# Performance work log

Measured on AMD Instinct MI355X. Metric: run time of the kernel, lower is better.

## Reference

```python
import jax, jax.numpy as jnp
import numpy as np

B, N, DE, H, DH = 2, 1024, 1024, 16, 64
DK = H * DH  # total complex qkv dim per stream
MIN_EXP = -30.0
EPS = 1e-4


def setup_inputs():
    key = jax.random.key(0)
    ks = jax.random.split(key, 8)

    def g(i, shape, sc=1.0):
        return jax.random.normal(ks[i], shape, jnp.float32) * sc

    # RoPE-style per-head frequencies for the conjugate-paired half-dims
    freqs = 10000.0 ** (-np.arange(DH // 2, dtype=np.float64) / (DH // 2))
    omega = jnp.asarray(np.tile(freqs[None, :], (H, 1)), jnp.float32)
    return {
        "x": g(0, (B, N, DE)),
        "Wq": g(1, (DE, 2 * DK), 1.0 / np.sqrt(DE)),
        "Wk": g(2, (DE, 2 * DK), 1.0 / np.sqrt(DE)),
        "Wv": g(3, (DE, 2 * DK), 1.0 / np.sqrt(DE)),
        "Wo": g(4, (2 * DK, DE), 1.0 / np.sqrt(2 * DK)),
        "omega": omega,
        "mu_raw": g(5, (H,)) - 2.0,          # pre-sigmoid decay rates
        "sigma_raw": g(6, (H,)),              # pre-softplus process noise
        "eta_raw": jnp.ones((H,), jnp.float32),
        "gamma_raw": jnp.ones((H,), jnp.float32),
        "tau": jnp.ones((H,), jnp.float32),   # inverse temperature
        "nu_raw": jnp.ones((H,), jnp.float32) * 4.0,  # robustness dof
    }


def reference(x, Wq, Wk, Wv, Wo, omega, mu_raw, sigma_raw, eta_raw, gamma_raw, tau, nu_raw):
    B_, N_, _ = x.shape
    H_, d_half = omega.shape
    DH_ = 2 * d_half
    DKt = H_ * DH_

    def cproj(W):
        z = x @ W                          # [B,N,2D] real/imag packed
        D = W.shape[1] // 2
        zc = jax.lax.complex(z[..., :D], z[..., D:])
        return zc.reshape(B_, N_, H_, DH_)

    q, k, v = cproj(Wq), cproj(Wk), cproj(Wv)

    # complex-conjugate-constrained rotations: omega stacked as [w, -w]
    om = jnp.concatenate([omega, -omega], axis=-1)              # [H,DH]
    t = jnp.arange(N_, dtype=jnp.float32)
    ang = t[:, None, None] * om[None]                           # [N,H,DH]
    phase = jax.lax.complex(jnp.cos(ang), jnp.sin(ang))
    qr = q * phase[None]
    kr = k * phase[None]

    # isotropic SDE decay kernel  E_rel = exp(-mu * |t_i - t_j|)
    mu = jax.nn.sigmoid(mu_raw) + EPS                           # [H]
    dt = jnp.abs(t[:, None] - t[None, :])                       # [N,N]
    E = jnp.exp(jnp.clip(-mu[:, None, None] * dt[None], MIN_EXP, 0.0))  # [H,N,N]

    # Re<q_i, Phi(dt) k_j>  (rotation carried by phases, decay by E)
    s = jnp.einsum('bihd,bjhd->bhij', qr, jnp.conj(kr)).real    # [B,H,N,N]
    qn = (q.real ** 2 + q.imag ** 2).sum(-1).transpose(0, 2, 1)  # [B,H,N]
    kn = (k.real ** 2 + k.imag ** 2).sum(-1).transpose(0, 2, 1)

    # Lyapunov-propagated uncertainty: P(dt) = sigma^2/(2mu)(1 - E^2) + eta^2 + gamma^2
    sigma_sq = jax.nn.softplus(sigma_raw)
    eta_sq = jax.nn.softplus(eta_raw)
    gamma_sq = jax.nn.softplus(gamma_raw)
    V = (sigma_sq / (2.0 * mu))[:, None, None] * (1.0 - E * E) \
        + (eta_sq + gamma_sq)[:, None, None]                    # [H,N,N]

    # per-head Mahalanobis residual under the SDE forecast
    maha = jnp.maximum(qn[..., None] + (E * E)[None] * kn[:, :, None, :]
                       - 2.0 * E[None] * s, 0.0) / V[None]      # [B,H,N,N]

    # robust nu-thresholding (Student-t style) + Gaussian normalization term
    nu = jax.nn.softplus(nu_raw)
    coef = (-0.5 * tau * (nu + DH_))[None, :, None, None]
    logits = coef * jnp.log1p(maha / nu[None, :, None, None]) \
             - 0.5 * DH_ * jnp.log(V)[None]

    causal = (t[:, None] >= t[None, :])
    logits = jnp.where(causal[None, None], logits, -jnp.inf)
    A = jax.nn.softmax(logits, axis=-1)                         # [B,H,N,N]

    out = jnp.einsum('bhij,bjhd->bihd', A.astype(v.dtype), v)   # complex [B,N,H,DH]
    y = jnp.concatenate([out.real.reshape(B_, N_, DKt),
                         out.imag.reshape(B_, N_, DKt)], axis=-1)
    return y @ Wo                                               # [B,N,DE]
```

## Files before the change

kernel.cpp:

```cpp
#include <hip/hip_runtime.h>
#include <math.h>

#define BB      2
#define NN      1024
#define DE_     1024
#define HH      16
#define TWO_DK  2048
#define PK      4194304
#define TBLR    1092

typedef float f32x4  __attribute__((ext_vector_type(4)));
typedef short bf16x8 __attribute__((ext_vector_type(8)));

__device__ __forceinline__ short f2bf(float f) {
    unsigned u = __float_as_uint(f);
    unsigned r = (u + 0x7fffu + ((u >> 16) & 1u)) >> 16;
    return (short)r;
}

#define GLDS16(g, l) __builtin_amdgcn_global_load_lds(                        \
    (const __attribute__((address_space(1))) unsigned int*)(g),               \
    (__attribute__((address_space(3))) unsigned int*)(l), 16, 0, 0)
#define GLDS4(g, l) __builtin_amdgcn_global_load_lds(                         \
    (const __attribute__((address_space(1))) unsigned int*)(g),               \
    (__attribute__((address_space(3))) unsigned int*)(l), 4, 0, 0)

__global__ __launch_bounds__(256) void prep(
    const float* __restrict__ x,
    const float* __restrict__ Wq, const float* __restrict__ Wk,
    const float* __restrict__ Wv, const float* __restrict__ Wo,
    const float* __restrict__ mu_raw, const float* __restrict__ sigma_raw,
    const float* __restrict__ eta_raw, const float* __restrict__ gamma_raw,
    short* __restrict__ xb, short* __restrict__ wt, short* __restrict__ wot,
    float4* __restrict__ tbl) {
    const int z = blockIdx.z;
    if (z == 4) {
        const int flat = blockIdx.y * 32 + blockIdx.x;
        const int i = (flat * 256 + threadIdx.x) * 8;
        float4 v0 = *(const float4*)&x[i];
        float4 v1 = *(const float4*)&x[i + 4];
        short4 o0, o1;
        o0.x = f2bf(v0.x); o0.y = f2bf(v0.y); o0.z = f2bf(v0.z); o0.w = f2bf(v0.w);
        o1.x = f2bf(v1.x); o1.y = f2bf(v1.y); o1.z = f2bf(v1.z); o1.w = f2bf(v1.w);
        *(short4*)&xb[i] = o0; *(short4*)&xb[i + 4] = o1;
        return;
    }
    if (z == 3 && blockIdx.x >= 16) {
        const int idx = blockIdx.y * 16 + (blockIdx.x - 16);
        if (idx >= 80) return;
        const int h = idx / 5, rb = idx % 5;
        const int r = rb * 256 + threadIdx.x;
        if (r >= TBLR) return;
        const float mu = 1.f / (1.f + expf(-mu_raw[h])) + 1e-4f;
        const float Ac = log1pf(expf(sigma_raw[h])) / (2.f * mu);
        const float Cc = log1pf(expf(eta_raw[h])) + log1pf(expf(gamma_raw[h]));
        const float arg = fminf(fmaxf(-mu * (float)(r - 64), -30.f), 0.f);
        const float E   = expf(arg);
        const float V   = fmaf(Ac, 1.f - E * E, Cc);
        tbl[h * TBLR + r] = make_float4(E, 1.f / V, -32.f * logf(V), 0.f);
        return;
    }
    const float* in; short* out; int R, C;
    if (z < 3) { if (blockIdx.y >= 16) return;
                 in = (z == 0) ? Wq : (z == 1) ? Wk : Wv;
                 out = wt + (size_t)z * 2097152; R = 1024; C = 2048; }
    else       { in = Wo; out = wot; R = 2048; C = 1024; }
    __shared__ float t[64][65];
    const int c0 = blockIdx.x * 64, r0 = blockIdx.y * 64;
    const int tr = threadIdx.x >> 4, tc4 = (threadIdx.x & 15) * 4;
#pragma unroll
    for (int s = 0; s < 4; ++s) {
        const int r = tr + s * 16;
        float4 v = *(const float4*)&in[(size_t)(r0 + r) * C + c0 + tc4];
        t[r][tc4] = v.x; t[r][tc4 + 1] = v.y; t[r][tc4 + 2] = v.z; t[r][tc4 + 3] = v.w;
    }
    __syncthreads();
#pragma unroll
    for (int s = 0; s < 4; ++s) {
        const int oc = tr + s * 16;
        short4 o;
        o.x = f2bf(t[tc4 + 0][oc]); o.y = f2bf(t[tc4 + 1][oc]);
        o.z = f2bf(t[tc4 + 2][oc]); o.w = f2bf(t[tc4 + 3][oc]);
        *(short4*)&out[(size_t)(c0 + oc) * R + r0 + tc4] = o;
    }
}

__global__ __launch_bounds__(256) void gemm_qkv_rot2(
    const short* __restrict__ A, const short* __restrict__ wt,
    const float* __restrict__ omega,
    short* __restrict__ qb, short* __restrict__ kb, short* __restrict__ vtb,
    float* __restrict__ qn_, float* __restrict__ kn_) {
    __shared__ __align__(16) short As[128 * 64];
    __shared__ __align__(16) short Bs[128 * 64];
    __shared__ float sN[2][128];
    const int tid = threadIdx.x;
    const int m0  = blockIdx.x * 128;
    const int h   = blockIdx.y;
    const short* W = wt + (size_t)blockIdx.z * 2097152;

    const short* aP[4]; const short* bP[4]; int ldsoff[4];
#pragma unroll
    for (int i = 0; i < 4; ++i) {
        const int c   = i * 256 + tid;
        const int row = c >> 3;
        const int src = ((c & 7) ^ (row & 7)) << 3;
        ldsoff[i] = c * 8;
        aP[i] = A + (size_t)(m0 + row) * 1024 + src;
        const int t_ = row >> 5, u_ = (row >> 4) & 1, dcol = t_ * 16 + (row & 15);
        bP[i] = W + (size_t)(u_ * 1024 + h * 64 + dcol) * 1024 + src;
    }

    const int lane = tid & 63, w = tid >> 6;
    const int wr = (w >> 1) * 64, hsel = w & 1, wc = hsel * 64;
    const int fr = lane & 15;
    const int fo = (lane >> 4) << 3;
    const int sw = (fr & 7) << 3;

    f32x4 acc[4][4];
#pragma unroll
    for (int a = 0; a < 4; ++a)
#pragma unroll
        for (int b = 0; b < 4; ++b) acc[a][b] = (f32x4){0.f, 0.f, 0.f, 0.f};

    for (int k0 = 0; k0 < 1024; k0 += 64) {
#pragma unroll
        for (int i = 0; i < 4; ++i) GLDS16(aP[i] + k0, &As[ldsoff[i]]);
#pragma unroll
        for (int i = 0; i < 4; ++i) GLDS16(bP[i] + k0, &Bs[ldsoff[i]]);
        __syncthreads();
#pragma unroll
        for (int ks = 0; ks < 64; ks += 32) {
            bf16x8 af[4], bf[4];
#pragma unroll
            for (int a = 0; a < 4; ++a)
                af[a] = *(const bf16x8*)&As[(wr + a * 16 + fr) * 64 + ((ks + fo) ^ sw)];
#pragma unroll
            for (int b = 0; b < 4; ++b)
                bf[b] = *(const bf16x8*)&Bs[(wc + b * 16 + fr) * 64 + ((ks + fo) ^ sw)];
#pragma unroll
            for (int a = 0; a < 4; ++a)
#pragma unroll
                for (int b = 0; b < 4; ++b)
                    acc[a][b] = __builtin_amdgcn_mfma_f32_16x16x32_bf16(
                        af[a], bf[b], acc[a][b], 0, 0, 0);
        }
        __syncthreads();
    }

    const int cq = (lane >> 4) * 4, l15 = lane & 15;
    const int bh  = (m0 >> 10) * 16 + h;
    const int nb0 = (m0 & 1023) + wr + cq;

    if (blockIdx.z == 2) {
#pragma unroll
        for (int a = 0; a < 4; ++a) {
#pragma unroll
            for (int b = 0; b < 4; ++b) {
                const int cl = wc + b * 16;
                const int dd = ((cl >> 4) & 1) * 64 + (cl >> 5) * 16 + l15;
                short4 o;
                o.x = f2bf(acc[a][b][0]); o.y = f2bf(acc[a][b][1]);
                o.z = f2bf(acc[a][b][2]); o.w = f2bf(acc[a][b][3]);
                *(short4*)&vtb[((size_t)bh * 128 + dd) * 1024 + nb0 + a * 16] = o;
            }
        }
        return;
    }
    float* nout = (blockIdx.z == 0) ? qn_ : kn_;
    short* obuf = (blockIdx.z == 0) ? qb  : kb;

#pragma unroll
    for (int a = 0; a < 4; ++a) {
        float ns[4] = {0.f, 0.f, 0.f, 0.f};
#pragma unroll
        for (int b = 0; b < 4; ++b)
#pragma unroll
            for (int r = 0; r < 4; ++r)
                ns[r] = fmaf(acc[a][b][r], acc[a][b][r], ns[r]);
#pragma unroll
        for (int m2 = 1; m2 < 16; m2 <<= 1)
#pragma unroll
            for (int r = 0; r < 4; ++r) ns[r] += __shfl_xor(ns[r], m2);
        if (l15 == 0)
#pragma unroll
            for (int r = 0; r < 4; ++r) sN[hsel][wr + a * 16 + cq + r] = ns[r];
    }
    __syncthreads();
    if (tid < 128)
        nout[(size_t)bh * 1024 + (m0 & 1023) + tid] = sN[0][tid] + sN[1][tid];

#pragma unroll
    for (int p = 0; p < 2; ++p) {
        const int d = (hsel * 2 + p) * 16 + l15;
        const float om = (d < 32) ? omega[h * 32 + d] : -omega[h * 32 + d - 32];
#pragma unroll
        for (int a = 0; a < 4; ++a) {
#pragma unroll
            for (int r = 0; r < 4; ++r) {
                const int n2 = nb0 + a * 16 + r;
                float sn, cs;
                __sincosf((float)n2 * om, &sn, &cs);
                const float re = acc[a][2 * p][r], im = acc[a][2 * p + 1][r];
                short* orow = obuf + ((size_t)bh * 1024 + n2) * 128;
                orow[d]      = f2bf(re * cs - im * sn);
                orow[64 + d] = f2bf(re * sn + im * cs);
            }
        }
    }
}

__global__ __launch_bounds__(256) void attn_mfma(
    const short* __restrict__ qr, const short* __restrict__ kr,
    const short* __restrict__ vt,
    const float* __restrict__ qn, const float* __restrict__ kn,
    const float4* __restrict__ tbl,
    const float* __restrict__ tau_p, const float* __restrict__ nu_raw,
    short* __restrict__ y) {
    __shared__ __align__(16) short Ks[2][64 * 128];
    __shared__ __align__(16) short Vs[2][128 * 64];
    __shared__ __align__(16) short Ps[64 * 72];
    __shared__ __align__(16) float4 sT[2][128];
    __shared__ float sKn[2][64];

    const int bx  = blockIdx.x;
    const int xcd = bx & 7;
    const int j   = bx >> 3;
    const int bh  = xcd * 4 + (j & 3);
    const int h   = bh & 15;
    const int itr = j >> 2;
    const int it  = (itr < 8) ? itr : 23 - itr;
    const int i0  = it * 64;
    const int tid  = threadIdx.x;
    const int lane = tid & 63, w = tid >> 6;
    const int quad = lane >> 4, l15 = lane & 15;

    const float nu     = log1pf(expf(nu_raw[h]));
    const float coef   = -0.5f * tau_p[h] * (nu + 64.0f);
    const float inv_nu = 1.f / nu;

    const short* Qb  = qr + (size_t)bh * NN * 128;
    const short* Kb  = kr + (size_t)bh * NN * 128;
    const short* Vtb = vt + (size_t)bh * 128 * NN;

#define STAGE(JT, P) do {                                                     \
        const int j0_ = (JT) * 64, dt0_ = i0 - j0_;                           \
        _Pragma("unroll")                                                     \
        for (int i_ = 0; i_ < 4; ++i_) {                                      \
            const int c_ = i_ * 256 + tid, row_ = c_ >> 4;                    \
            const int src_ = ((c_ & 15) ^ (row_ & 7)) * 8;                    \
            GLDS16(Kb + (size_t)(j0_ + row_) * 128 + src_, &Ks[P][c_ * 8]);   \
        }                                                                     \
        _Pragma("unroll")                                                     \
        for (int i_ = 0; i_ < 4; ++i_) {                                      \
            const int c_ = i_ * 256 + tid, d_ = c_ >> 3;                      \
            const int src_ = ((c_ & 7) ^ (d_ & 7)) * 8;                       \
            GLDS16(Vtb + (size_t)d_ * NN + j0_ + src_, &Vs[P][c_ * 8]);       \
        }                                                                     \
        if (w == 0) {                                                         \
            GLDS16(tbl + h * TBLR + 1 + dt0_ + lane, &sT[P][lane]);           \
            GLDS16(tbl + h * TBLR + 65 + dt0_ + lane, &sT[P][64 + lane]);     \
        } else if (w == 1) {                                                  \
            GLDS4(kn + (size_t)bh * NN + j0_ + lane, &sKn[P][lane]);          \
        }                                                                     \
    } while (0)

    bf16x8 qf[4];
    const int arow = i0 + w * 16 + l15;
#pragma unroll
    for (int ks = 0; ks < 4; ++ks)
        qf[ks] = *(const bf16x8*)&Qb[(size_t)arow * 128 + ks * 32 + quad * 8];

    float mrow[4], lrow[4];
    f32x4 o[8];
#pragma unroll
    for (int r = 0; r < 4; ++r) { mrow[r] = -INFINITY; lrow[r] = 0.f; }
#pragma unroll
    for (int s = 0; s < 8; ++s) o[s] = (f32x4){0.f, 0.f, 0.f, 0.f};
    float qn4[4];
#pragma unroll
    for (int r = 0; r < 4; ++r)
        qn4[r] = qn[(size_t)bh * NN + i0 + w * 16 + quad * 4 + r];

    STAGE(0, 0);
    __syncthreads();

    for (int jt = 0; jt <= it; ++jt) {
        const int p = jt & 1;
        if (jt < it) STAGE(jt + 1, 1 - p);

        f32x4 sAcc[4];
#pragma unroll
        for (int s = 0; s < 4; ++s) sAcc[s] = (f32x4){0.f, 0.f, 0.f, 0.f};
#pragma unroll
        for (int ks = 0; ks < 4; ++ks) {
#pragma unroll
            for (int s = 0; s < 4; ++s) {
                const int brow = s * 16 + l15;
                bf16x8 bK = *(const bf16x8*)&Ks[p][brow * 128 +
                                                  (((ks * 4 + quad) ^ (brow & 7)) * 8)];
                sAcc[s] = __builtin_amdgcn_mfma_f32_16x16x32_bf16(qf[ks], bK, sAcc[s], 0, 0, 0);
            }
        }

        float al[4];
#pragma unroll
        for (int r = 0; r < 4; ++r) {
            const int row = w * 16 + quad * 4 + r;
            float lg[4];
            float mx = -INFINITY;
#pragma unroll
            for (int s = 0; s < 4; ++s) {
                const int col = s * 16 + l15;
                const float4 T = sT[p][row - col + 63];
                const float sv = sAcc[s][r];
                const float maha =
                    fmaxf(fmaf(T.x * T.x, sKn[p][col], qn4[r]) - 2.f * T.x * sv, 0.f) * T.y;
                float v = fmaf(coef, __logf(fmaf(maha, inv_nu, 1.f)), T.z);
                if (jt == it && col > row) v = -INFINITY;
                lg[s] = v;
                mx = fmaxf(mx, v);
            }
            mx = fmaxf(mx, __shfl_xor(mx, 1));
            mx = fmaxf(mx, __shfl_xor(mx, 2));
            mx = fmaxf(mx, __shfl_xor(mx, 4));
            mx = fmaxf(mx, __shfl_xor(mx, 8));
            const float mn = fmaxf(mrow[r], mx);
            const float a_ = __expf(mrow[r] - mn);
            float rs = 0.f;
#pragma unroll
            for (int s = 0; s < 4; ++s) {
                const float pv = __expf(lg[s] - mn);
                Ps[row * 72 + s * 16 + l15] = f2bf(pv);
                rs += pv;
            }
            rs += __shfl_xor(rs, 1);
            rs += __shfl_xor(rs, 2);
            rs += __shfl_xor(rs, 4);
            rs += __shfl_xor(rs, 8);
            lrow[r] = fmaf(lrow[r], a_, rs);
            mrow[r] = mn;
            al[r] = a_;
        }
#pragma unroll
        for (int s = 0; s < 8; ++s)
#pragma unroll
            for (int r = 0; r < 4; ++r) o[s][r] *= al[r];

#pragma unroll
        for (int jc = 0; jc < 2; ++jc) {
            bf16x8 aP = *(const bf16x8*)&Ps[(w * 16 + l15) * 72 + jc * 32 + quad * 8];
#pragma unroll
            for (int sub = 0; sub < 8; ++sub) {
                const int d = sub * 16 + l15;
                bf16x8 bV = *(const bf16x8*)&Vs[p][d * 64 + (((jc * 4 + quad) ^ (d & 7)) * 8)];
                o[sub] = __builtin_amdgcn_mfma_f32_16x16x32_bf16(aP, bV, o[sub], 0, 0, 0);
            }
        }
        if (jt < it) __syncthreads();
    }
#undef STAGE

#pragma unroll
    for (int r = 0; r < 4; ++r) {
        const float inv = 1.f / lrow[r];
        const size_t base = ((size_t)bh * NN + i0 + w * 16 + quad * 4 + r) * 128;
#pragma unroll
        for (int sub = 0; sub < 8; ++sub)
            y[base + sub * 16 + l15] = f2bf(o[sub][r] * inv);
    }
}

__global__ __launch_bounds__(256) void gemm_out64(
    const short* __restrict__ yb, const short* __restrict__ wot,
    float* __restrict__ out) {
    __shared__ __align__(16) short As[64 * 64];
    __shared__ __align__(16) short Bs[64 * 64];
    const int tid = threadIdx.x;
    const int m0  = blockIdx.x * 64;
    const int n0  = blockIdx.y * 64;
    const int bb  = m0 >> 10;

    int aPre[2], aOff[2]; const short* bP[2];
#pragma unroll
    for (int i = 0; i < 2; ++i) {
        const int c = i * 256 + tid, row = c >> 3;
        const int src = ((c & 7) ^ (row & 7)) << 3;
        aPre[i] = ((m0 & 1023) + row) * 128 + src;
        bP[i] = wot + (size_t)(n0 + row) * 2048 + src;
        aOff[i] = c * 8;
    }

    const int lane = tid & 63, w = tid >> 6;
    const int wr = (w >> 1) * 32, wc = (w & 1) * 32;
    const int fr = lane & 15;
    const int fo = (lane >> 4) << 3;
    const int sw = (fr & 7) << 3;

    f32x4 acc[2][2];
#pragma unroll
    for (int a = 0; a < 2; ++a)
#pragma unroll
        for (int b = 0; b < 2; ++b) acc[a][b] = (f32x4){0.f, 0.f, 0.f, 0.f};

    for (int k0 = 0; k0 < 2048; k0 += 64) {
        const int hh = (k0 >> 6) & 15, im = k0 >> 10;
        const short* ab = yb + ((size_t)(bb * 16 + hh) << 17) + im * 64;
#pragma unroll
        for (int i = 0; i < 2; ++i) GLDS16(ab + aPre[i], &As[aOff[i]]);
#pragma unroll
        for (int i = 0; i < 2; ++i) GLDS16(bP[i] + k0, &Bs[aOff[i]]);
        __syncthreads();
#pragma unroll
        for (int ks = 0; ks < 64; ks += 32) {
            bf16x8 af[2], bf[2];
#pragma unroll
            for (int a = 0; a < 2; ++a)
                af[a] = *(const bf16x8*)&As[(wr + a * 16 + fr) * 64 + ((ks + fo) ^ sw)];
#pragma unroll
            for (int b = 0; b < 2; ++b)
                bf[b] = *(const bf16x8*)&Bs[(wc + b * 16 + fr) * 64 + ((ks + fo) ^ sw)];
#pragma unroll
            for (int a = 0; a < 2; ++a)
#pragma unroll
                for (int b = 0; b < 2; ++b)
                    acc[a][b] = __builtin_amdgcn_mfma_f32_16x16x32_bf16(
                        af[a], bf[b], acc[a][b], 0, 0, 0);
        }
        __syncthreads();
    }

    const int cq = (lane >> 4) * 4, l15 = lane & 15;
#pragma unroll
    for (int a = 0; a < 2; ++a)
#pragma unroll
        for (int b = 0; b < 2; ++b)
#pragma unroll
            for (int r = 0; r < 4; ++r)
                out[(size_t)(m0 + wr + a * 16 + cq + r) * 1024 +
                    (n0 + wc + b * 16 + l15)] = acc[a][b][r];
}

extern "C" void kernel_launch(void* const* d_in, const int* in_sizes, int n_in,
                              void* d_out, int out_size, void* d_ws, size_t ws_size,
                              hipStream_t stream) {
    const float* x         = (const float*)d_in[0];
    const float* Wq        = (const float*)d_in[1];
    const float* Wk        = (const float*)d_in[2];
    const float* Wv        = (const float*)d_in[3];
    const float* Wo        = (const float*)d_in[4];
    const float* omega     = (const float*)d_in[5];
    const float* mu_raw    = (const float*)d_in[6];
    const float* sigma_raw = (const float*)d_in[7];
    const float* eta_raw   = (const float*)d_in[8];
    const float* gamma_raw = (const float*)d_in[9];
    const float* tau       = (const float*)d_in[10];
    const float* nu_raw    = (const float*)d_in[11];
    float* out = (float*)d_out;

    short*  qb  = (short*)d_ws;
    short*  kb  = qb + PK;
    short*  vtb = kb + PK;
    float*  qn  = (float*)(vtb + PK);
    float*  kn  = qn + 32768;
    float4* tbl = (float4*)(kn + 32768);
    short*  wot = (short*)(tbl + HH * TBLR);
    short*  wt  = wot + 2097152;
    short*  xb  = wt + 3 * 2097152;
    short*  yb  = wt;

    prep<<<dim3(32, 32, 5), 256, 0, stream>>>(
        x, Wq, Wk, Wv, Wo, mu_raw, sigma_raw, eta_raw, gamma_raw,
        xb, wt, wot, tbl);
    gemm_qkv_rot2<<<dim3(16, 16, 3), 256, 0, stream>>>(
        xb, wt, omega, qb, kb, vtb, qn, kn);
    attn_mfma<<<dim3(512), 256, 0, stream>>>(
        qb, kb, vtb, qn, kn, tbl, tau, nu_raw, yb);
    gemm_out64<<<dim3(32, 16), 256, 0, stream>>>(yb, wot, out);
}
```

Baseline: 216.7 us.

## Pair high and low 32-row query tiles per attention block for causal balance

Each attention block now handles two 32-row query tiles, one near the end of the sequence and its mirror near the start, packed into the 64-row MFMA layout. The goal is to even out causal work across blocks so they all run a similar number of key tiles, instead of relying on the earlier tile-order permutation. Rows from the low tile stop their softmax updates once past their causal range and write zeros into P. The MFMA work on those wasted rows is still issued, and the table staging and masking logic become more complex.

```diff
diff --git a/kernel.cpp b/kernel.cpp
--- a/kernel.cpp
+++ b/kernel.cpp
@@ -219,7 +219,7 @@
     __shared__ __align__(16) short Ks[2][64 * 128];
     __shared__ __align__(16) short Vs[2][128 * 64];
     __shared__ __align__(16) short Ps[64 * 72];
-    __shared__ __align__(16) float4 sT[2][128];
+    __shared__ __align__(16) float4 sT[2][192];
     __shared__ float sKn[2][64];
 
     const int bx  = blockIdx.x;
@@ -228,11 +228,19 @@
     const int bh  = xcd * 4 + (j & 3);
     const int h   = bh & 15;
     const int itr = j >> 2;
-    const int it  = (itr < 8) ? itr : 23 - itr;
-    const int i0  = it * 64;
+    const int fi  = (itr < 8) ? itr : 23 - itr;
+    const int i0h = (31 - fi) * 32;
+    const int i0l = fi * 32;
+    const int jtHi = (31 - fi) >> 1;
+    const int jtLo = fi >> 1;
+
     const int tid  = threadIdx.x;
     const int lane = tid & 63, w = tid >> 6;
     const int quad = lane >> 4, l15 = lane & 15;
+    const int hi   = (quad < 2);
+    const int lrg  = w * 8 + (quad & 1) * 4;
+    const int i0g  = hi ? i0h : i0l;
+    const int goff = hi ? 0 : 96;
 
     const float nu     = log1pf(expf(nu_raw[h]));
     const float coef   = -0.5f * tau_p[h] * (nu + 64.0f);
@@ -243,7 +251,7 @@
     const short* Vtb = vt + (size_t)bh * 128 * NN;
 
 #define STAGE(JT, P) do {                                                     \
-        const int j0_ = (JT) * 64, dt0_ = i0 - j0_;                           \
+        const int j0_ = (JT) * 64;                                            \
         _Pragma("unroll")                                                     \
         for (int i_ = 0; i_ < 4; ++i_) {                                      \
             const int c_ = i_ * 256 + tid, row_ = c_ >> 4;                    \
@@ -257,15 +265,22 @@
             GLDS16(Vtb + (size_t)d_ * NN + j0_ + src_, &Vs[P][c_ * 8]);       \
         }                                                                     \
         if (w == 0) {                                                         \
-            GLDS16(tbl + h * TBLR + 1 + dt0_ + lane, &sT[P][lane]);           \
-            GLDS16(tbl + h * TBLR + 65 + dt0_ + lane, &sT[P][64 + lane]);     \
+            const float4* tb_ = tbl + h * TBLR + 1 + i0h - j0_;               \
+            GLDS16(tb_ + lane, &sT[P][lane]);                                 \
+            if (lane < 32) GLDS16(tb_ + 64 + lane, &sT[P][64 + lane]);        \
         } else if (w == 1) {                                                  \
+            if ((JT) <= jtLo) {                                               \
+                const float4* tb_ = tbl + h * TBLR + 1 + i0l - j0_;           \
+                GLDS16(tb_ + lane, &sT[P][96 + lane]);                        \
+                if (lane < 32) GLDS16(tb_ + 64 + lane, &sT[P][160 + lane]);   \
+            }                                                                 \
+        } else if (w == 2) {                                                  \
             GLDS4(kn + (size_t)bh * NN + j0_ + lane, &sKn[P][lane]);          \
         }                                                                     \
     } while (0)
 
     bf16x8 qf[4];
-    const int arow = i0 + w * 16 + l15;
+    const int arow = (l15 < 8) ? (i0h + w * 8 + l15) : (i0l + w * 8 + (l15 - 8));
 #pragma unroll
     for (int ks = 0; ks < 4; ++ks)
         qf[ks] = *(const bf16x8*)&Qb[(size_t)arow * 128 + ks * 32 + quad * 8];
@@ -279,14 +294,14 @@
     float qn4[4];
 #pragma unroll
     for (int r = 0; r < 4; ++r)
-        qn4[r] = qn[(size_t)bh * NN + i0 + w * 16 + quad * 4 + r];
+        qn4[r] = qn[(size_t)bh * NN + i0g + lrg + r];
 
     STAGE(0, 0);
     __syncthreads();
 
-    for (int jt = 0; jt <= it; ++jt) {
+    for (int jt = 0; jt <= jtHi; ++jt) {
         const int p = jt & 1;
-        if (jt < it) STAGE(jt + 1, 1 - p);
+        if (jt < jtHi) STAGE(jt + 1, 1 - p);
 
         f32x4 sAcc[4];
 #pragma unroll
@@ -303,43 +318,60 @@
         }
 
         float al[4];
-#pragma unroll
-        for (int r = 0; r < 4; ++r) {
-            const int row = w * 16 + quad * 4 + r;
-            float lg[4];
-            float mx = -INFINITY;
-#pragma unroll
-            for (int s = 0; s < 4; ++s) {
-                const int col = s * 16 + l15;
-                const float4 T = sT[p][row - col + 63];
-                const float sv = sAcc[s][r];
-                const float maha =
-                    fmaxf(fmaf(T.x * T.x, sKn[p][col], qn4[r]) - 2.f * T.x * sv, 0.f) * T.y;
-                float v = fmaf(coef, __logf(fmaf(maha, inv_nu, 1.f)), T.z);
-                if (jt == it && col > row) v = -INFINITY;
-                lg[s] = v;
-                mx = fmaxf(mx, v);
+        if (hi || jt <= jtLo) {
+            const int lastT = hi ? (jt == jtHi) : (jt == jtLo);
+            const int dt0g  = i0g - jt * 64;
+#pragma unroll
+            for (int r = 0; r < 4; ++r) {
+                const int prow  = w * 16 + quad * 4 + r;
+                const int lrowg = lrg + r;
+                float lg[4];
+                float mx = -INFINITY;
+#pragma unroll
+                for (int s = 0; s < 4; ++s) {
+                    const int scol = s * 16 + l15;
+                    const float4 T = sT[p][goff + lrowg - scol + 63];
+                    const float sv = sAcc[s][r];
+                    const float maha =
+                        fmaxf(fmaf(T.x * T.x, sKn[p][scol], qn4[r]) - 2.f * T.x * sv, 0.f) * T.y;
+                    float v = fmaf(coef, __logf(fmaf(maha, inv_nu, 1.f)), T.z);
+                    if (lastT && scol > dt0g + lrowg) v = -INFINITY;
+                    lg[s] = v;
+                    mx = fmaxf(mx, v);
+                }
+                mx = fmaxf(mx, __shfl_xor(mx, 1));
+                mx = fmaxf(mx, __shfl_xor(mx, 2));
+                mx = fmaxf(mx, __shfl_xor(mx, 4));
+                mx = fmaxf(mx, __shfl_xor(mx, 8));
+                const float mn = fmaxf(mrow[r], mx);
+                const float a_ = __expf(mrow[r] - mn);
+                float rs = 0.f;
+#pragma unroll
+                for (int s = 0; s < 4; ++s) {
+                    const float pv = __expf(lg[s] - mn);
+                    Ps[prow * 72 + s * 16 + l15] = f2bf(pv);
+                    rs += pv;
+                }
+                rs += __shfl_xor(rs, 1);
+                rs += __shfl_xor(rs, 2);
+                rs += __shfl_xor(rs, 4);
+                rs += __shfl_xor(rs, 8);
+                lrow[r] = fmaf(lrow[r], a_, rs);
+                mrow[r] = mn;
+                al[r] = a_;
             }
-            mx = fmaxf(mx, __shfl_xor(mx, 1));
-            mx = fmaxf(mx, __shfl_xor(mx, 2));
-            mx = fmaxf(mx, __shfl_xor(mx, 4));
-            mx = fmaxf(mx, __shfl_xor(mx, 8));
-            const float mn = fmaxf(mrow[r], mx);
-            const float a_ = __expf(mrow[r] - mn);
-            float rs = 0.f;
-#pragma unroll
-            for (int s = 0; s < 4; ++s) {
-                const float pv = __expf(lg[s] - mn);
-                Ps[row * 72 + s * 16 + l15] = f2bf(pv);
-                rs += pv;
+        } else {
+#pragma unroll
+            for (int r = 0; r < 4; ++r) al[r] = 1.f;
+            if (jt == jtLo + 1) {
+#pragma unroll
+                for (int r = 0; r < 4; ++r) {
+                    const int prow = w * 16 + quad * 4 + r;
+#pragma unroll
+                    for (int s = 0; s < 4; ++s)
+                        Ps[prow * 72 + s * 16 + l15] = 0;
+                }
             }
-            rs += __shfl_xor(rs, 1);
-            rs += __shfl_xor(rs, 2);
-            rs += __shfl_xor(rs, 4);
-            rs += __shfl_xor(rs, 8);
-            lrow[r] = fmaf(lrow[r], a_, rs);
-            mrow[r] = mn;
-            al[r] = a_;
         }
 #pragma unroll
         for (int s = 0; s < 8; ++s)
@@ -356,14 +388,14 @@
                 o[sub] = __builtin_amdgcn_mfma_f32_16x16x32_bf16(aP, bV, o[sub], 0, 0, 0);
             }
         }
-        if (jt < it) __syncthreads();
+        if (jt < jtHi) __syncthreads();
     }
 #undef STAGE
 
 #pragma unroll
     for (int r = 0; r < 4; ++r) {
         const float inv = 1.f / lrow[r];
-        const size_t base = ((size_t)bh * NN + i0 + w * 16 + quad * 4 + r) * 128;
+        const size_t base = ((size_t)bh * NN + i0g + lrg + r) * 128;
 #pragma unroll
         for (int sub = 0; sub < 8; ++sub)
             y[base + sub * 16 + l15] = f2bf(o[sub][r] * inv);
```

Measured after the change: 223.5 us. +3.2%, slower.

## Use base-2 softmax with lazy rescaling and MFMA row sums in attention

Applied to the files above, without the earlier changes.

Moves the attention logits and softmax into the base-2 domain using hardware exp2/log2 intrinsics. The table now stores 2E and E² so the Mahalanobis term needs fewer multiplies. The running max is only rescaled when it grows by more than 16, which skips most output rescales. Row sums come from an extra MFMA against a ones vector instead of shuffle reductions. The block-to-(head, tile) mapping also changes, which alters how causal work is balanced across workgroups. The trade-off is an extra MFMA per chunk and larger unnormalised probability values stored in bf16.

```diff
diff --git a/kernel.cpp b/kernel.cpp
--- a/kernel.cpp
+++ b/kernel.cpp
@@ -17,6 +17,9 @@
     unsigned r = (u + 0x7fffu + ((u >> 16) & 1u)) >> 16;
     return (short)r;
 }
+
+__device__ __forceinline__ float fexp2(float x) { return __builtin_amdgcn_exp2f(x); }
+__device__ __forceinline__ float flog2(float x) { return __builtin_amdgcn_logf(x); }
 
 #define GLDS16(g, l) __builtin_amdgcn_global_load_lds(                        \
     (const __attribute__((address_space(1))) unsigned int*)(g),               \
@@ -57,7 +60,7 @@
         const float arg = fminf(fmaxf(-mu * (float)(r - 64), -30.f), 0.f);
         const float E   = expf(arg);
         const float V   = fmaf(Ac, 1.f - E * E, Cc);
-        tbl[h * TBLR + r] = make_float4(E, 1.f / V, -32.f * logf(V), 0.f);
+        tbl[h * TBLR + r] = make_float4(2.f * E, 1.f / V, -32.f * log2f(V), E * E);
         return;
     }
     const float* in; short* out; int R, C;
@@ -225,11 +228,13 @@
     const int bx  = blockIdx.x;
     const int xcd = bx & 7;
     const int j   = bx >> 3;
-    const int bh  = xcd * 4 + (j & 3);
+    const int b2  = j & 3;
+    const int itr = j >> 2;
+    const int bh  = xcd * 4 + (b2 & 1) * 2 + (itr >> 3);
     const int h   = bh & 15;
-    const int itr = j >> 2;
-    const int it  = (itr < 8) ? itr : 23 - itr;
+    const int it  = ((itr & 7) << 1) | (b2 >> 1);
     const int i0  = it * 64;
+
     const int tid  = threadIdx.x;
     const int lane = tid & 63, w = tid >> 6;
     const int quad = lane >> 4, l15 = lane & 15;
@@ -270,16 +275,20 @@
     for (int ks = 0; ks < 4; ++ks)
         qf[ks] = *(const bf16x8*)&Qb[(size_t)arow * 128 + ks * 32 + quad * 8];
 
-    float mrow[4], lrow[4];
+    float mrow[4];
     f32x4 o[8];
-#pragma unroll
-    for (int r = 0; r < 4; ++r) { mrow[r] = -INFINITY; lrow[r] = 0.f; }
+    f32x4 o9 = (f32x4){0.f, 0.f, 0.f, 0.f};
+#pragma unroll
+    for (int r = 0; r < 4; ++r) mrow[r] = -INFINITY;
 #pragma unroll
     for (int s = 0; s < 8; ++s) o[s] = (f32x4){0.f, 0.f, 0.f, 0.f};
     float qn4[4];
 #pragma unroll
     for (int r = 0; r < 4; ++r)
         qn4[r] = qn[(size_t)bh * NN + i0 + w * 16 + quad * 4 + r];
+
+    const bf16x8 onesv = (bf16x8){0x3F80, 0x3F80, 0x3F80, 0x3F80,
+                                  0x3F80, 0x3F80, 0x3F80, 0x3F80};
 
     STAGE(0, 0);
     __syncthreads();
@@ -303,48 +312,46 @@
         }
 
         float al[4];
+        bool anyr = false;
 #pragma unroll
         for (int r = 0; r < 4; ++r) {
             const int row = w * 16 + quad * 4 + r;
             float lg[4];
-            float mx = -INFINITY;
 #pragma unroll
             for (int s = 0; s < 4; ++s) {
                 const int col = s * 16 + l15;
                 const float4 T = sT[p][row - col + 63];
                 const float sv = sAcc[s][r];
-                const float maha =
-                    fmaxf(fmaf(T.x * T.x, sKn[p][col], qn4[r]) - 2.f * T.x * sv, 0.f) * T.y;
-                float v = fmaf(coef, __logf(fmaf(maha, inv_nu, 1.f)), T.z);
+                const float t1 = fmaf(T.w, sKn[p][col], qn4[r]);
+                const float maha = fmaxf(fmaf(-T.x, sv, t1), 0.f) * T.y;
+                float v = fmaf(coef, flog2(fmaf(maha, inv_nu, 1.f)), T.z);
                 if (jt == it && col > row) v = -INFINITY;
                 lg[s] = v;
-                mx = fmaxf(mx, v);
-            }
+            }
+            float mx = fmaxf(fmaxf(lg[0], lg[1]), fmaxf(lg[2], lg[3]));
             mx = fmaxf(mx, __shfl_xor(mx, 1));
             mx = fmaxf(mx, __shfl_xor(mx, 2));
             mx = fmaxf(mx, __shfl_xor(mx, 4));
             mx = fmaxf(mx, __shfl_xor(mx, 8));
-            const float mn = fmaxf(mrow[r], mx);
-            const float a_ = __expf(mrow[r] - mn);
-            float rs = 0.f;
+            const bool resc = mx > mrow[r] + 16.f;
+            const float mu_ = resc ? mx : mrow[r];
+            al[r] = resc ? fexp2(mrow[r] - mx) : 1.f;
+            mrow[r] = mu_;
+            anyr = anyr || resc;
 #pragma unroll
             for (int s = 0; s < 4; ++s) {
-                const float pv = __expf(lg[s] - mn);
+                const float pv = fexp2(lg[s] - mu_);
                 Ps[row * 72 + s * 16 + l15] = f2bf(pv);
-                rs += pv;
-            }
-            rs += __shfl_xor(rs, 1);
-            rs += __shfl_xor(rs, 2);
-            rs += __shfl_xor(rs, 4);
-            rs += __shfl_xor(rs, 8);
-            lrow[r] = fmaf(lrow[r], a_, rs);
-            mrow[r] = mn;
-            al[r] = a_;
-        }
-#pragma unroll
-        for (int s = 0; s < 8; ++s)
-#pragma unroll
-            for (int r = 0; r < 4; ++r) o[s][r] *= al[r];
+            }
+        }
+        if (anyr) {
+#pragma unroll
+            for (int s = 0; s < 8; ++s)
+#pragma unroll
+                for (int r = 0; r < 4; ++r) o[s][r] *= al[r];
+#pragma unroll
+            for (int r = 0; r < 4; ++r) o9[r] *= al[r];
+        }
 
 #pragma unroll
         for (int jc = 0; jc < 2; ++jc) {
@@ -355,6 +362,7 @@
                 bf16x8 bV = *(const bf16x8*)&Vs[p][d * 64 + (((jc * 4 + quad) ^ (d & 7)) * 8)];
                 o[sub] = __builtin_amdgcn_mfma_f32_16x16x32_bf16(aP, bV, o[sub], 0, 0, 0);
             }
+            o9 = __builtin_amdgcn_mfma_f32_16x16x32_bf16(aP, onesv, o9, 0, 0, 0);
         }
         if (jt < it) __syncthreads();
     }
@@ -362,7 +370,7 @@
 
 #pragma unroll
     for (int r = 0; r < 4; ++r) {
-        const float inv = 1.f / lrow[r];
+        const float inv = 1.f / o9[r];
         const size_t base = ((size_t)bh * NN + i0 + w * 16 + quad * 4 + r) * 128;
 #pragma unroll
         for (int sub = 0; sub < 8; ++sub)
```

After: 210.9 us. 1.03x faster.
